# Optimization experiments

Measured on AMD Instinct MI355X. Metric: run time of the kernel, lower is better.

Reference implementation:

```python
import jax, jax.numpy as jnp
import numpy as np

N = 4096
IN_DIM = 128
OUT_DIM = 64
LEAKY_SLOPE = 0.2


def setup_inputs() -> dict:
    key = jax.random.key(0)
    ks = jax.random.split(key, 8)
    H = jax.random.normal(ks[0], (N, IN_DIM), dtype=jnp.float32)
    # dense 0/1 adjacency per relation (int constants w.r.t. autodiff)
    A_buys = jax.random.randint(ks[1], (N, N), 0, 2, dtype=jnp.int32)
    A_views = jax.random.randint(ks[2], (N, N), 0, 2, dtype=jnp.int32)
    # xavier_uniform for W (stored [in, out]; Wh = H @ W == torch Linear with weight W.T)
    s_w = float(np.sqrt(6.0 / (IN_DIM + OUT_DIM)))
    W_buys = jax.random.uniform(ks[3], (IN_DIM, OUT_DIM), jnp.float32, -s_w, s_w)
    W_views = jax.random.uniform(ks[4], (IN_DIM, OUT_DIM), jnp.float32, -s_w, s_w)
    # xavier_uniform on a.view(1, 2*out_dim)
    s_a = float(np.sqrt(6.0 / (1 + 2 * OUT_DIM)))
    a_buys = jax.random.uniform(ks[5], (2 * OUT_DIM,), jnp.float32, -s_a, s_a)
    a_views = jax.random.uniform(ks[6], (2 * OUT_DIM,), jnp.float32, -s_a, s_a)
    bias = jnp.zeros((OUT_DIM,), dtype=jnp.float32)
    return {"H": H, "A_buys": A_buys, "A_views": A_views,
            "W_buys": W_buys, "W_views": W_views,
            "a_buys": a_buys, "a_views": a_views, "bias": bias}


def _relation(H, A, W, a):
    Wh = H @ W                                  # [N, OUT]
    # (cat(Wh_i, Wh_j) * a).sum(-1) == Wh_i @ a[:OUT] + Wh_j @ a[OUT:]
    s_i = Wh @ a[:OUT_DIM]                      # [N]
    s_j = Wh @ a[OUT_DIM:]                      # [N]
    e = jax.nn.leaky_relu(s_i[:, None] + s_j[None, :], LEAKY_SLOPE)  # [N, N]
    e = jnp.where(A == 0, -jnp.inf, e)
    alpha = jnp.nan_to_num(jax.nn.softmax(e, axis=1))                # isolated rows -> 0
    return alpha @ Wh                           # [N, OUT]


def reference(H, A_buys, A_views, W_buys, W_views, a_buys, a_views, bias):
    agg = _relation(H, A_buys, W_buys, a_buys) + _relation(H, A_views, W_views, a_views)
    return agg + bias
```

## Files before the change

### kernel.cpp

```cpp
#include <hip/hip_runtime.h>

#define NN 4096
#define IND 128
#define OUTD 64
#define WJ 128
#define NWIN 8
#define LOG2E 1.44269504088896340736f

typedef __attribute__((ext_vector_type(4))) float  floatx4;
typedef __attribute__((ext_vector_type(8))) __bf16 bf16x8;
typedef __attribute__((ext_vector_type(4))) int    intx4;

#if __has_builtin(__builtin_amdgcn_exp2f)
#define EXP2(x) __builtin_amdgcn_exp2f(x)
#else
#define EXP2(x) exp2f(x)
#endif

__device__ __forceinline__ unsigned short f2bf(float f) {
  unsigned int u = __float_as_uint(f);
  u += 0x7fffu + ((u >> 16) & 1u);
  return (unsigned short)(u >> 16);
}

__global__ __launch_bounds__(256) void gat_prep(
    const float* __restrict__ H,
    const int* __restrict__ A0, const int* __restrict__ A1,
    const float* __restrict__ W0, const float* __restrict__ W1,
    const float* __restrict__ av0, const float* __restrict__ av1,
    unsigned short* __restrict__ whF,
    float* __restrict__ sA, float* __restrict__ sB,
    unsigned* __restrict__ PW)
{
  const int rel = blockIdx.y;
  const int t = threadIdx.x;

  if (blockIdx.x >= 256) {
    const int cb = blockIdx.x - 256;
    const int* __restrict__ Ar = rel ? A1 : A0;
    unsigned* __restrict__ pwr = PW + (size_t)rel * NN * 128;
    __shared__ unsigned char nib[2][4][256];
    for (int rr = 0; rr < 2; rr++) {
      const int row = cb * 2 + rr;
      const int* __restrict__ ap = Ar + (size_t)row * NN;
#pragma unroll
      for (int it = 0; it < 4; it++) {
        intx4 a = *(const intx4*)(ap + it * 1024 + t * 4);
        nib[rr][it][t] = (unsigned char)((a[0] != 0) | ((a[1] != 0) << 1) |
                                         ((a[2] != 0) << 2) | ((a[3] != 0) << 3));
      }
      __syncthreads();
      if (t < 128) {
        const int wq = t >> 5, lj = t & 31;
        unsigned wd = 0;
#pragma unroll
        for (int v = 0; v < 8; v++)
          wd |= (unsigned)nib[rr][wq][v * 32 + lj] << (4 * v);
        pwr[(size_t)row * 128 + t] = wd;
      }
    }
    return;
  }

  const float* __restrict__ W  = rel ? W1 : W0;
  const float* __restrict__ av = rel ? av1 : av0;
  const int i0 = blockIdx.x * 16;
  const int c = t & 63;
  const int wv = __builtin_amdgcn_readfirstlane(t >> 6);
  const float* __restrict__ hp = H + (size_t)(i0 + wv * 4) * IND;

  float acc0 = 0.f, acc1 = 0.f, acc2 = 0.f, acc3 = 0.f;
#pragma unroll 8
  for (int k = 0; k < IND; k += 4) {
    float4 h0 = *(const float4*)(hp + k);
    float4 h1 = *(const float4*)(hp + IND + k);
    float4 h2 = *(const float4*)(hp + 2 * IND + k);
    float4 h3 = *(const float4*)(hp + 3 * IND + k);
    float w0 = W[(k + 0) * OUTD + c];
    float w1 = W[(k + 1) * OUTD + c];
    float w2 = W[(k + 2) * OUTD + c];
    float w3 = W[(k + 3) * OUTD + c];
    acc0 += h0.x * w0 + h0.y * w1 + h0.z * w2 + h0.w * w3;
    acc1 += h1.x * w0 + h1.y * w1 + h1.z * w2 + h1.w * w3;
    acc2 += h2.x * w0 + h2.y * w1 + h2.z * w2 + h2.w * w3;
    acc3 += h3.x * w0 + h3.y * w1 + h3.z * w2 + h3.w * w3;
  }

  const float alo = av[c] * LOG2E, ahi = av[OUTD + c] * LOG2E;
  float pa0 = acc0 * alo, pa1 = acc1 * alo, pa2 = acc2 * alo, pa3 = acc3 * alo;
  float pb0 = acc0 * ahi, pb1 = acc1 * ahi, pb2 = acc2 * ahi, pb3 = acc3 * ahi;
#pragma unroll
  for (int off = 32; off >= 1; off >>= 1) {
    pa0 += __shfl_xor(pa0, off); pa1 += __shfl_xor(pa1, off);
    pa2 += __shfl_xor(pa2, off); pa3 += __shfl_xor(pa3, off);
    pb0 += __shfl_xor(pb0, off); pb1 += __shfl_xor(pb1, off);
    pb2 += __shfl_xor(pb2, off); pb3 += __shfl_xor(pb3, off);
  }
  const int ibase = i0 + wv * 4;
  if (c == 0) {
    float* sa = sA + rel * NN + ibase;
    float* sb = sB + rel * NN + ibase;
    sa[0] = pa0; sa[1] = pa1; sa[2] = pa2; sa[3] = pa3;
    sb[0] = pb0; sb[1] = pb1; sb[2] = pb2; sb[3] = pb3;
  }

  unsigned long long packed =
      (unsigned long long)f2bf(acc0)        | ((unsigned long long)f2bf(acc1) << 16) |
      ((unsigned long long)f2bf(acc2) << 32) | ((unsigned long long)f2bf(acc3) << 48);
  *(unsigned long long*)(whF + ((size_t)(rel * 512 + (ibase >> 3)) * 64 + c) * 8 + (ibase & 7)) = packed;
}

__global__ __launch_bounds__(512, 2) void gat_fused(
    const unsigned* __restrict__ PW,
    const unsigned short* __restrict__ whF,
    const float* __restrict__ sA, const float* __restrict__ sB,
    const float* __restrict__ bias,
    float* __restrict__ out)
{
  __shared__ char lds[8][2][4096];
  const int i0   = blockIdx.x * 16;
  const int t    = threadIdx.x;
  const int w    = t >> 6;
  const int rel  = w >> 2;
  const int lane = t & 63;
  const int quad = lane >> 4;
  const int m    = lane & 15;
  const int lj   = lane & 31;
  const int half = lane >> 5;
  const int s_st = lj >> 1;
  const int wboff = s_st * 256 + (lj & 1) * 8;
  const unsigned short* __restrict__ wh = whF + (size_t)rel * 512 * 64 * 8;
  const float* __restrict__ sbp = sB + rel * NN;

  float si_r[8];
#pragma unroll
  for (int p = 0; p < 8; p++) si_r[p] = sA[rel * NN + i0 + 2 * p + half];

  unsigned pw[8];
  const unsigned* __restrict__ pwp =
      PW + ((size_t)(rel * NN + i0 + half) * 4 + (w & 3)) * 32 + lj;
#pragma unroll
  for (int p = 0; p < 8; p++) pw[p] = pwp[(size_t)(2 * p) * 128];

  const int jbase = (w & 3) * (NWIN * WJ);

  floatx4 acc0 = {0.f,0.f,0.f,0.f}, acc1 = acc0, acc2 = acc0, acc3 = acc0, acc4 = acc0;
  bf16x8 vone;
#pragma unroll
  for (int k = 0; k < 8; k++) vone[k] = (__bf16)1.0f;

  float4 sjv2[2];
  bf16x8 b[4][4];

  auto issueS = [&](int win) {
    sjv2[win & 1] = *(const float4*)(sbp + jbase + win * WJ + lj * 4);
  };

  auto stage = [&](int win) {
    char* slice = lds[w][win & 1];
    const float4 sjv = sjv2[win & 1];
#pragma unroll
    for (int p = 0; p < 8; p++) {
      const int rp = 2 * p + half;
      const float si = si_r[p];
      const unsigned nb = (pw[p] >> (win * 4)) & 0xFu;
      float t0 = si + sjv.x, t1 = si + sjv.y, t2 = si + sjv.z, t3 = si + sjv.w;
      float e0 = EXP2(fmaxf(t0, 0.2f * t0));
      float e1 = EXP2(fmaxf(t1, 0.2f * t1));
      float e2 = EXP2(fmaxf(t2, 0.2f * t2));
      float e3 = EXP2(fmaxf(t3, 0.2f * t3));
      e0 = (nb & 1u) ? e0 : 0.f;
      e1 = (nb & 2u) ? e1 : 0.f;
      e2 = (nb & 4u) ? e2 : 0.f;
      e3 = (nb & 8u) ? e3 : 0.f;
      uint2 pk;
      pk.x = (unsigned)f2bf(e0) | ((unsigned)f2bf(e1) << 16);
      pk.y = (unsigned)f2bf(e2) | ((unsigned)f2bf(e3) << 16);
      *(uint2*)(slice + wboff + ((rp ^ s_st) & 15) * 16) = pk;
    }
  };

  auto issueB = [&](int win) {
    const int jw = jbase + win * WJ;
    const unsigned short* bb = wh + ((size_t)(jw >> 3) + quad) * 512 + (size_t)m * 8;
#pragma unroll
    for (int ks = 0; ks < 4; ks++)
#pragma unroll
      for (int nt = 0; nt < 4; nt++)
        b[ks][nt] = *(const bf16x8*)(bb + (size_t)ks * 2048 + nt * 128);
  };

  auto domfma = [&](int win) {
    char* slice = lds[w][win & 1];
    bf16x8 afr[4];
#pragma unroll
    for (int ks = 0; ks < 4; ks++) {
      const int s = ks * 4 + quad;
      afr[ks] = *(const bf16x8*)(slice + s * 256 + ((m ^ s) & 15) * 16);
    }
#pragma unroll
    for (int ks = 0; ks < 4; ks++) {
      acc0 = __builtin_amdgcn_mfma_f32_16x16x32_bf16(afr[ks], b[ks][0], acc0, 0, 0, 0);
      acc1 = __builtin_amdgcn_mfma_f32_16x16x32_bf16(afr[ks], b[ks][1], acc1, 0, 0, 0);
      acc2 = __builtin_amdgcn_mfma_f32_16x16x32_bf16(afr[ks], b[ks][2], acc2, 0, 0, 0);
      acc3 = __builtin_amdgcn_mfma_f32_16x16x32_bf16(afr[ks], b[ks][3], acc3, 0, 0, 0);
      acc4 = __builtin_amdgcn_mfma_f32_16x16x32_bf16(afr[ks], vone,     acc4, 0, 0, 0);
    }
  };

  issueS(0); issueS(1);
  stage(0);

#pragma unroll
  for (int win = 0; win < NWIN; win++) {
    issueB(win);
    if (win + 2 < NWIN) issueS(win + 2);
    if (win + 1 < NWIN) stage(win + 1);
    domfma(win);
  }

  float* redw  = (float*)lds[w][0];
  float* dredw = (float*)lds[w][1];
#pragma unroll
  for (int r = 0; r < 4; r++) {
    const int row = quad * 4 + r;
    redw[row * 64 + 0 * 16 + m] = acc0[r];
    redw[row * 64 + 1 * 16 + m] = acc1[r];
    redw[row * 64 + 2 * 16 + m] = acc2[r];
    redw[row * 64 + 3 * 16 + m] = acc3[r];
  }
  if (m == 0) {
#pragma unroll
    for (int r = 0; r < 4; r++) dredw[quad * 4 + r] = acc4[r];
  }
  __syncthreads();

  const int c  = t & 63;
  const int r0 = t >> 6;
  const float bc = bias[c];
#pragma unroll
  for (int rr = r0; rr < 16; rr += 8) {
    float n0 = 0.f, n1 = 0.f, d0 = 0.f, d1 = 0.f;
#pragma unroll
    for (int ww = 0; ww < 4; ww++) {
      n0 += ((const float*)lds[ww][0])[rr * 64 + c];
      d0 += ((const float*)lds[ww][1])[rr];
      n1 += ((const float*)lds[ww + 4][0])[rr * 64 + c];
      d1 += ((const float*)lds[ww + 4][1])[rr];
    }
    const float inv0 = d0 > 0.f ? 1.f / d0 : 0.f;
    const float inv1 = d1 > 0.f ? 1.f / d1 : 0.f;
    out[(size_t)(i0 + rr) * OUTD + c] = n0 * inv0 + n1 * inv1 + bc;
  }
}

extern "C" void kernel_launch(void* const* d_in, const int* in_sizes, int n_in,
                              void* d_out, int out_size, void* d_ws, size_t ws_size,
                              hipStream_t stream) {
  const float* H    = (const float*)d_in[0];
  const int*   A0   = (const int*)d_in[1];
  const int*   A1   = (const int*)d_in[2];
  const float* W0   = (const float*)d_in[3];
  const float* W1   = (const float*)d_in[4];
  const float* av0  = (const float*)d_in[5];
  const float* av1  = (const float*)d_in[6];
  const float* bias = (const float*)d_in[7];
  float* out = (float*)d_out;

  const size_t whF_b = (size_t)2 * 512 * 64 * 8 * 2;
  const size_t s_b   = (size_t)2 * NN * 4;

  unsigned short* whF = (unsigned short*)d_ws;
  float*          sA  = (float*)((char*)d_ws + whF_b);
  float*          sB  = (float*)((char*)d_ws + whF_b + s_b);
  unsigned*       PW  = (unsigned*)((char*)d_ws + whF_b + 2 * s_b);

  gat_prep<<<dim3(256 + 2048, 2), 256, 0, stream>>>(H, A0, A1, W0, W1, av0, av1,
                                                    whF, sA, sB, PW);
  gat_fused<<<NN / 16, 512, 0, stream>>>(PW, whF, sA, sB, bias, out);
}
```

Measured before the change: 184.3 us.

## Batch eight adjacency rows per block with register double-buffered nontemporal loads

The adjacency bit-packing blocks now process eight rows each. The next pair of rows is prefetched into registers with nontemporal loads while the current pair is packed into a double-buffered shared tile, and all 256 threads write packed words. This aims to keep more memory requests in flight and to cut block-launch and sync overhead for the bandwidth-bound adjacency read. In exchange it uses more registers and launches fewer blocks.

```diff
diff --git a/kernel.cpp b/kernel.cpp
--- a/kernel.cpp
+++ b/kernel.cpp
@@ -39,25 +39,49 @@
     const int cb = blockIdx.x - 256;
     const int* __restrict__ Ar = rel ? A1 : A0;
     unsigned* __restrict__ pwr = PW + (size_t)rel * NN * 128;
-    __shared__ unsigned char nib[2][4][256];
+    const int r0 = cb * 8;
+    __shared__ unsigned char nib[2][2][4][256];
+    intx4 av[2][2][4];
+
+#pragma unroll
     for (int rr = 0; rr < 2; rr++) {
-      const int row = cb * 2 + rr;
-      const int* __restrict__ ap = Ar + (size_t)row * NN;
-#pragma unroll
-      for (int it = 0; it < 4; it++) {
-        intx4 a = *(const intx4*)(ap + it * 1024 + t * 4);
-        nib[rr][it][t] = (unsigned char)((a[0] != 0) | ((a[1] != 0) << 1) |
-                                         ((a[2] != 0) << 2) | ((a[3] != 0) << 3));
+      const int* ap = Ar + (size_t)(r0 + rr) * NN + t * 4;
+#pragma unroll
+      for (int s = 0; s < 4; s++)
+        av[0][rr][s] = __builtin_nontemporal_load((const intx4*)(ap + s * 1024));
+    }
+
+#pragma unroll
+    for (int it = 0; it < 4; it++) {
+      const int buf = it & 1;
+      if (it < 3) {
+#pragma unroll
+        for (int rr = 0; rr < 2; rr++) {
+          const int* ap = Ar + (size_t)(r0 + 2 * (it + 1) + rr) * NN + t * 4;
+#pragma unroll
+          for (int s = 0; s < 4; s++)
+            av[buf ^ 1][rr][s] =
+                __builtin_nontemporal_load((const intx4*)(ap + s * 1024));
+        }
       }
+#pragma unroll
+      for (int rr = 0; rr < 2; rr++)
+#pragma unroll
+        for (int s = 0; s < 4; s++) {
+          intx4 a = av[buf][rr][s];
+          nib[buf][rr][s][t] =
+              (unsigned char)((a[0] != 0) | ((a[1] != 0) << 1) |
+                              ((a[2] != 0) << 2) | ((a[3] != 0) << 3));
+        }
       __syncthreads();
-      if (t < 128) {
-        const int wq = t >> 5, lj = t & 31;
-        unsigned wd = 0;
-#pragma unroll
-        for (int v = 0; v < 8; v++)
-          wd |= (unsigned)nib[rr][wq][v * 32 + lj] << (4 * v);
-        pwr[(size_t)row * 128 + t] = wd;
-      }
+      const int rr   = t >> 7;
+      const int wd_i = t & 127;
+      const int wq = wd_i >> 5, lj = wd_i & 31;
+      unsigned wd = 0;
+#pragma unroll
+      for (int v = 0; v < 8; v++)
+        wd |= (unsigned)nib[buf][rr][wq][v * 32 + lj] << (4 * v);
+      pwr[(size_t)(r0 + 2 * it + rr) * 128 + wd_i] = wd;
     }
     return;
   }
@@ -275,7 +299,7 @@
   float*          sB  = (float*)((char*)d_ws + whF_b + s_b);
   unsigned*       PW  = (unsigned*)((char*)d_ws + whF_b + 2 * s_b);
 
-  gat_prep<<<dim3(256 + 2048, 2), 256, 0, stream>>>(H, A0, A1, W0, W1, av0, av1,
-                                                    whF, sA, sB, PW);
+  gat_prep<<<dim3(256 + 512, 2), 256, 0, stream>>>(H, A0, A1, W0, W1, av0, av1,
+                                                   whF, sA, sB, PW);
   gat_fused<<<NN / 16, 512, 0, stream>>>(PW, whF, sA, sB, bias, out);
 }
```

Measured after the change: 178.8 us. 1.03x faster.
